# Optimization experiments

Measured on AMD Instinct MI355X. Metric: run time of the kernel, lower is better.

The kernel has to match this reference:

```python
import jax, jax.numpy as jnp
import numpy as np

N_QUBITS = 18
LAYERS = 6
DATA_REUPLOADING = True


def _apply_1q(state, gate, q, n):
    # state: [2^n] complex, gate: [2,2] complex, acts on qubit q (big-endian)
    s = state.reshape(2 ** q, 2, 2 ** (n - q - 1))
    s = jnp.einsum('ab,ibj->iaj', gate, s)
    return s.reshape(-1)


def _apply_cz_adj(state, q, n):
    # CZ on adjacent qubits (q, q+1): flip sign of |..11..> amplitudes
    s = state.reshape(2 ** q, 2, 2, 2 ** (n - q - 2))
    s = s.at[:, 1, 1, :].multiply(-1.0)
    return s.reshape(-1)


def _rx(t):
    c = jnp.cos(t / 2).astype(jnp.complex64)
    s = (-1j * jnp.sin(t / 2)).astype(jnp.complex64)
    return jnp.stack([jnp.stack([c, s]), jnp.stack([s, c])])


def _ry(t):
    c = jnp.cos(t / 2).astype(jnp.complex64)
    s = jnp.sin(t / 2).astype(jnp.complex64)
    return jnp.stack([jnp.stack([c, -s]), jnp.stack([s, c])])


def _rz(t):
    em = jnp.exp(-1j * t.astype(jnp.complex64) / 2)
    ep = jnp.exp(1j * t.astype(jnp.complex64) / 2)
    z = jnp.zeros((), jnp.complex64)
    return jnp.stack([jnp.stack([em, z]), jnp.stack([z, ep])])


def _circuit(x, input_scaling, variational):
    # Hardware-efficient ansatz: RX(data) encoding, RY+RZ variational, CZ chain
    n = N_QUBITS
    state = jnp.zeros(2 ** n, jnp.complex64).at[0].set(1.0)
    for l in range(LAYERS):
        if l == 0 or DATA_REUPLOADING:
            for q in range(n):
                state = _apply_1q(state, _rx(input_scaling[l, q] * x[q]), q, n)
        for q in range(n):
            state = _apply_1q(state, _ry(variational[l, q]), q, n)
        for q in range(n):
            state = _apply_1q(state, _rz(variational[l, n + q]), q, n)
        for q in range(n - 1):
            state = _apply_cz_adj(state, q, n)
    return state


def setup_inputs() -> dict:
    key = jax.random.key(0)
    k1, k2, k3 = jax.random.split(key, 3)
    x1 = jax.random.normal(k1, (N_QUBITS,), jnp.float32)
    x2 = jax.random.normal(k2, (N_QUBITS,), jnp.float32)
    input_scaling = jnp.ones((LAYERS, N_QUBITS), jnp.float32)
    variational = (jax.random.uniform(k3, (LAYERS, 2 * N_QUBITS), jnp.float32)
                   * 2 * np.pi - np.pi)
    return {"x1": x1, "x2": x2, "input_scaling": input_scaling,
            "variational": variational}


def reference(x1, x2, input_scaling, variational):
    psi1 = _circuit(x1, input_scaling, variational)
    psi2 = _circuit(x2, input_scaling, variational)
    # projector |0><0| expectation of U(x2)^dagger U(x1)|0> == |<psi2|psi1>|^2
    ov = jnp.vdot(psi2, psi1)
    return (ov.real ** 2 + ov.imag ** 2).astype(jnp.float32)
```

## Files before the change

### kernel.cpp

```cpp
#include <hip/hip_runtime.h>
#include <math.h>


#define NQ      18
#define NSTATE  (1 << NQ)
#define TPB     256

__device__ __forceinline__ int SW(int i) { return i ^ ((i >> 5) & 31); }

__device__ __forceinline__ float2 cmulf(float2 a, float2 b) {
    return make_float2(a.x * b.x - a.y * b.y, a.x * b.y + a.y * b.x);
}

__device__ __forceinline__ void compose_U(double cx, double sx, double cy,
                                          double sy, double zc, double zs,
                                          float2* up)
{
    double m00r = cy * cx,  m00i =  sy * sx;
    double m01r = -sy * cx, m01i = -cy * sx;
    double m10r = sy * cx,  m10i = -cy * sx;
    double m11r = cy * cx,  m11i = -sy * sx;
    up[0] = make_float2((float)(m00r * zc + m00i * zs), (float)(m00i * zc - m00r * zs));
    up[1] = make_float2((float)(m01r * zc + m01i * zs), (float)(m01i * zc - m01r * zs));
    up[2] = make_float2((float)(m10r * zc - m10i * zs), (float)(m10i * zc + m10r * zs));
    up[3] = make_float2((float)(m11r * zc - m11i * zs), (float)(m11i * zc + m11r * zs));
}

__device__ __forceinline__ void cpair(
    float& a0r, float& a0i, float& a1r, float& a1i,
    float u00r, float u00i, float u01r, float u01i,
    float u10r, float u10i, float u11r, float u11i)
{
    float n0r = u00r * a0r - u00i * a0i + u01r * a1r - u01i * a1i;
    float n0i = u00r * a0i + u00i * a0r + u01r * a1i + u01i * a1r;
    float n1r = u10r * a0r - u10i * a0i + u11r * a1r - u11i * a1i;
    float n1i = u10r * a0i + u10i * a0r + u11r * a1i + u11i * a1r;
    a0r = n0r; a0i = n0i; a1r = n1r; a1i = n1i;
}

template<int RB>
__device__ __forceinline__ void reg_gate8(float (&ar)[8], float (&ai)[8],
                                          const float2* up)
{
    float u00r = up[0].x, u00i = up[0].y, u01r = up[1].x, u01i = up[1].y;
    float u10r = up[2].x, u10i = up[2].y, u11r = up[3].x, u11i = up[3].y;
#pragma unroll
    for (int r = 0; r < 8; ++r) {
        if (r & RB) continue;
        int r1 = r | RB;
        cpair(ar[r], ai[r], ar[r1], ai[r1],
              u00r, u00i, u01r, u01i, u10r, u10i, u11r, u11i);
    }
}

__device__ __forceinline__ void lane_gate8(float (&ar)[8], float (&ai)[8],
                                           const float2* up, int lane, int j)
{
    float u00r = up[0].x, u00i = up[0].y, u01r = up[1].x, u01i = up[1].y;
    float u10r = up[2].x, u10i = up[2].y, u11r = up[3].x, u11i = up[3].y;
    int side = (lane >> j) & 1;
    float car = side ? u11r : u00r, cai = side ? u11i : u00i;
    float cbr = side ? u10r : u01r, cbi = side ? u10i : u01i;
#pragma unroll
    for (int r = 0; r < 8; ++r) {
        float pr = __shfl_xor(ar[r], 1 << j, 64);
        float pi = __shfl_xor(ai[r], 1 << j, 64);
        float mr = ar[r], mi = ai[r];
        ar[r] = car * mr - cai * mi + cbr * pr - cbi * pi;
        ai[r] = car * mi + cai * mr + cbr * pi + cbi * pr;
    }
}

__global__ __launch_bounds__(TPB) void sim_kernel(
    float2* __restrict__ states,
    const float* __restrict__ x1, const float* __restrict__ x2,
    const float* __restrict__ iscale, const float* __restrict__ var,
    double* __restrict__ acc, unsigned* __restrict__ cnt)
{
    __shared__ float sre[2048], sim_[2048];
    __shared__ float2 sUa[5 * 11 * 4];
    __shared__ float2 sUb[5 * 11 * 4];
    __shared__ float2 sDa[6 * 4];
    __shared__ float2 sDb[11 * 4];

    int blk = blockIdx.x, t = threadIdx.x, lane = t & 63, wave = t >> 6;
    int c = blk >> 7, gc = blk & 127;
    const float* xv = c ? x2 : x1;

    if (blk == 0 && t == 0) { acc[0] = 0.0; acc[1] = 0.0; *cnt = 0u; }

    if (t < 110) {
        int which = t >= 55;
        int tt = which ? t - 55 : t;
        int l = tt / 11, w = tt % 11;
        int q = which ? (17 - w) : (10 - w);
        double tx = (double)iscale[l * NQ + q] * (double)xv[q];
        double ty = (double)var[l * 2 * NQ + q];
        double tz = (double)var[l * 2 * NQ + NQ + q];
        double sx, cx, sy, cy, sz, cz;
        sincos(tx * 0.5, &sx, &cx);
        sincos(ty * 0.5, &sy, &cy);
        sincos(tz * 0.5, &sz, &cz);
        compose_U(cx, sx, cy, sy, cz, sz,
                  which ? &sUb[(l * 11 + w) * 4] : &sUa[(l * 11 + w) * 4]);
    } else if (t < 127) {
        int isb = t >= 116;
        int j = isb ? (t - 116) : (t - 110);
        int q = isb ? (17 - j) : (5 - j);
        double d = (double)iscale[5 * NQ + q] * ((double)x1[q] - (double)x2[q]);
        double sn, cs;
        sincos(d * 0.5, &sn, &cs);
        float2* up = isb ? &sDb[j * 4] : &sDa[j * 4];
        up[0] = make_float2((float)cs, 0.f);  up[1] = make_float2(0.f, (float)-sn);
        up[2] = make_float2(0.f, (float)-sn); up[3] = make_float2((float)cs, 0.f);
    }
    __syncthreads();

    float ar[8], ai[8];
    auto W1 = [&](int r) { return r | (wave << 3) | (lane << 5); };
    auto W2 = [&](int r) { return wave | (r << 2) | (lane << 5); };
    auto X1 = [&](int r) { return lane | (wave << 6) | (r << 8); };
    auto X2 = [&](int r) { return lane | (r << 6) | (wave << 9); };
    auto rot = [&](auto from, auto to) {
#pragma unroll
        for (int r = 0; r < 8; ++r) { int s = SW(from(r)); sre[s] = ar[r]; sim_[s] = ai[r]; }
        __syncthreads();
#pragma unroll
        for (int r = 0; r < 8; ++r) { int s = SW(to(r)); ar[r] = sre[s]; ai[r] = sim_[s]; }
    };
    auto Ua = [&](int l, int w) -> const float2* { return &sUa[(l * 11 + w) * 4]; };
    auto Ub = [&](int l, int w) -> const float2* { return &sUb[(l * 11 + w) * 4]; };
    auto czfold = [&](unsigned M, auto gidx) {
#pragma unroll
        for (int r = 0; r < 8; ++r) {
            int i = gidx(r);
            if (__popc(i & (i >> 1) & M) & 1) { ar[r] = -ar[r]; ai[r] = -ai[r]; }
        }
    };
    auto g1_1 = [&](int r) { return W1(r) << 7; };
    auto g1_2 = [&](int r) { return W2(r) << 7; };
    auto g2_1 = [&](int r) { return (gc << 11) | X1(r); };
    auto g2_2 = [&](int r) { return (gc << 11) | X2(r); };

    {
        float2 com = make_float2(1.f, 0.f);
        const float2* u3 = Ua(0, 3); com = cmulf(com, (wave & 1) ? u3[2] : u3[0]);
        const float2* u4 = Ua(0, 4); com = cmulf(com, (wave >> 1) ? u4[2] : u4[0]);
#pragma unroll
        for (int j = 0; j < 6; ++j) {
            const float2* u = Ua(0, 5 + j);
            com = cmulf(com, ((lane >> j) & 1) ? u[2] : u[0]);
        }
        const float2* u0 = Ua(0, 0); const float2* u1 = Ua(0, 1); const float2* u2 = Ua(0, 2);
#pragma unroll
        for (int r = 0; r < 8; ++r) {
            float2 f = cmulf((r & 1) ? u0[2] : u0[0], (r & 2) ? u1[2] : u1[0]);
            f = cmulf(f, (r & 4) ? u2[2] : u2[0]);
            f = cmulf(com, f);
            ar[r] = f.x; ai[r] = f.y;
        }
    }
    czfold(0x1FF80u, g1_1);
    reg_gate8<2>(ar, ai, Ua(1, 1));
    reg_gate8<4>(ar, ai, Ua(1, 2));
#pragma unroll
    for (int j = 0; j < 6; ++j) lane_gate8(ar, ai, Ua(1, 5 + j), lane, j);
    rot(W1, W2);
    reg_gate8<2>(ar, ai, Ua(1, 3));
    reg_gate8<4>(ar, ai, Ua(1, 4));
    czfold(0x1FF00u, g1_2);
    reg_gate8<1>(ar, ai, Ua(2, 2));
    reg_gate8<2>(ar, ai, Ua(2, 3));
    reg_gate8<4>(ar, ai, Ua(2, 4));
#pragma unroll
    for (int j = 0; j < 6; ++j) lane_gate8(ar, ai, Ua(2, 5 + j), lane, j);
    rot(W2, W1);
    czfold(0x1FE00u, g1_1);
#pragma unroll
    for (int j = 0; j < 6; ++j) lane_gate8(ar, ai, Ua(3, 5 + j), lane, j);
    rot(W1, W2);
    reg_gate8<2>(ar, ai, Ua(3, 3));
    reg_gate8<4>(ar, ai, Ua(3, 4));
    czfold(0x1FC00u, g1_2);
    reg_gate8<4>(ar, ai, Ua(4, 4));
#pragma unroll
    for (int j = 0; j < 6; ++j) lane_gate8(ar, ai, Ua(4, 5 + j), lane, j);
    rot(W2, W1);
    czfold(0x1F800u, g1_1);
    if (c == 0) {
#pragma unroll
        for (int j = 0; j < 6; ++j) lane_gate8(ar, ai, &sDa[j * 4], lane, j);
    }
#pragma unroll
    for (int r = 0; r < 8; ++r) { int s = SW(W1(r)); sre[s] = ar[r]; sim_[s] = ai[r]; }
    __syncthreads();
#pragma unroll
    for (int r = 0; r < 8; ++r) {
        int x = X1(r);
        if ((x & 127) == 0) {
            int Wv = (gc << 4) | (x >> 7);
            int s = SW(Wv);
            ar[r] = sre[s]; ai[r] = sim_[s];
        } else { ar[r] = 0.f; ai[r] = 0.f; }
    }
    __syncthreads();

#pragma unroll
    for (int j = 0; j < 6; ++j) lane_gate8(ar, ai, Ub(0, j), lane, j);
    rot(X1, X2);
    reg_gate8<1>(ar, ai, Ub(0, 6));
    czfold(0x7Fu, g2_2);
#pragma unroll
    for (int j = 0; j < 6; ++j) lane_gate8(ar, ai, Ub(1, j), lane, j);
    reg_gate8<1>(ar, ai, Ub(1, 6));
    reg_gate8<2>(ar, ai, Ub(1, 7));
    rot(X2, X1);
    czfold(0xFFu, g2_1);
#pragma unroll
    for (int j = 0; j < 6; ++j) lane_gate8(ar, ai, Ub(2, j), lane, j);
    reg_gate8<1>(ar, ai, Ub(2, 8));
    rot(X1, X2);
    reg_gate8<1>(ar, ai, Ub(2, 6));
    reg_gate8<2>(ar, ai, Ub(2, 7));
    czfold(0x1FFu, g2_2);
#pragma unroll
    for (int j = 0; j < 6; ++j) lane_gate8(ar, ai, Ub(3, j), lane, j);
    reg_gate8<1>(ar, ai, Ub(3, 6));
    reg_gate8<2>(ar, ai, Ub(3, 7));
    reg_gate8<4>(ar, ai, Ub(3, 8));
    rot(X2, X1);
    reg_gate8<2>(ar, ai, Ub(3, 9));
    czfold(0x3FFu, g2_1);
#pragma unroll
    for (int j = 0; j < 6; ++j) lane_gate8(ar, ai, Ub(4, j), lane, j);
    reg_gate8<1>(ar, ai, Ub(4, 8));
    reg_gate8<2>(ar, ai, Ub(4, 9));
    reg_gate8<4>(ar, ai, Ub(4, 10));
    czfold(0x71Fu, g2_1);
    if (c == 0) {
#pragma unroll
        for (int j = 0; j < 5; ++j) lane_gate8(ar, ai, &sDb[j * 4], lane, j);
        reg_gate8<2>(ar, ai, &sDb[9 * 4]);
        reg_gate8<4>(ar, ai, &sDb[10 * 4]);
    }
    rot(X1, X2);
    reg_gate8<1>(ar, ai, Ub(4, 6));
    reg_gate8<2>(ar, ai, Ub(4, 7));
    czfold(0xE0u, g2_2);
    if (c == 0) {
        lane_gate8(ar, ai, &sDb[5 * 4], lane, 5);
        reg_gate8<1>(ar, ai, &sDb[6 * 4]);
        reg_gate8<2>(ar, ai, &sDb[7 * 4]);
        reg_gate8<4>(ar, ai, &sDb[8 * 4]);
    }
    float2* st = states + (size_t)c * NSTATE;
#pragma unroll
    for (int r = 0; r < 8; ++r) {
        int i = (gc << 11) | X2(r);
        st[i] = make_float2(ar[r], ai[r]);
    }
}

__global__ __launch_bounds__(TPB) void dot_kernel(
    const float2* __restrict__ states,
    const float* __restrict__ x1, const float* __restrict__ x2,
    const float* __restrict__ iscale,
    double* __restrict__ acc, unsigned* __restrict__ cnt,
    float* __restrict__ out)
{
    __shared__ double wr[4], wi[4];
    int t = threadIdx.x, lane = t & 63, wave = t >> 6;
    const float2* s1 = states;
    const float2* s2 = states + NSTATE;

    double d = (double)iscale[5 * NQ + 6] * ((double)x1[6] - (double)x2[6]);
    double sn, cs;
    sincos(d * 0.5, &sn, &cs);
    float cf = (float)cs, sf = (float)sn;

    int base = (blockIdx.x * TPB + t) * 4;
    int pbase = base ^ 2048;
    double accr = 0.0, acci = 0.0;
#pragma unroll
    for (int k = 0; k < 4; ++k) {
        float2 p1 = s1[base + k], pp = s1[pbase + k], p2 = s2[base + k];
        float gr = cf * p1.x + sf * pp.y;
        float gi = cf * p1.y - sf * pp.x;
        accr += (double)p2.x * gr + (double)p2.y * gi;
        acci += (double)p2.x * gi - (double)p2.y * gr;
    }
    for (int o = 32; o > 0; o >>= 1) {
        accr += __shfl_down(accr, o, 64);
        acci += __shfl_down(acci, o, 64);
    }
    if (lane == 0) { wr[wave] = accr; wi[wave] = acci; }
    __syncthreads();
    if (t == 0) {
        double br = wr[0] + wr[1] + wr[2] + wr[3];
        double bi = wi[0] + wi[1] + wi[2] + wi[3];
        atomicAdd(&acc[0], br);
        atomicAdd(&acc[1], bi);
        __threadfence();
        unsigned old = atomicAdd(cnt, 1u);
        if (old == gridDim.x - 1) {
            double fr = atomicAdd(&acc[0], 0.0);
            double fi = atomicAdd(&acc[1], 0.0);
            out[0] = (float)(fr * fr + fi * fi);
        }
    }
}

extern "C" void kernel_launch(void* const* d_in, const int* in_sizes, int n_in,
                              void* d_out, int out_size, void* d_ws, size_t ws_size,
                              hipStream_t stream)
{
    const float* x1 = (const float*)d_in[0];
    const float* x2 = (const float*)d_in[1];
    const float* iscale = (const float*)d_in[2];
    const float* var = (const float*)d_in[3];
    float* out = (float*)d_out;

    double*   acc    = (double*)((char*)d_ws + 8192);
    unsigned* cnt    = (unsigned*)((char*)d_ws + 8320);
    float2*   states = (float2*)((char*)d_ws + 16384);

    sim_kernel<<<256, TPB, 0, stream>>>(states, x1, x2, iscale, var, acc, cnt);
    dot_kernel<<<NSTATE / (TPB * 4), TPB, 0, stream>>>(states, x1, x2, iscale,
                                                       acc, cnt, out);
}
```

Before: 100.2 us.

## Fuse overlap reduction into sim kernel via inter-block flag synchronization

```diff
diff --git a/kernel.cpp b/kernel.cpp
--- a/kernel.cpp
+++ b/kernel.cpp
@@ -5,6 +5,7 @@
 #define NQ      18
 #define NSTATE  (1 << NQ)
 #define TPB     256
+#define MAGIC   0x5EED5EEDu
 
 __device__ __forceinline__ int SW(int i) { return i ^ ((i >> 5) & 31); }
 
@@ -23,7 +24,7 @@
     up[0] = make_float2((float)(m00r * zc + m00i * zs), (float)(m00i * zc - m00r * zs));
     up[1] = make_float2((float)(m01r * zc + m01i * zs), (float)(m01i * zc - m01r * zs));
     up[2] = make_float2((float)(m10r * zc - m10i * zs), (float)(m10i * zc + m10r * zs));
-    up[3] = make_float2((float)(m11r * zc - m11i * zs), (float)(m11i * zc + m11r * zs));
+    up[3] = make_float2((float)(m11r * zc + m11i * zs), (float)(m11i * zc + m11r * zs));
 }
 
 __device__ __forceinline__ void cpair(
@@ -75,19 +76,26 @@
     float2* __restrict__ states,
     const float* __restrict__ x1, const float* __restrict__ x2,
     const float* __restrict__ iscale, const float* __restrict__ var,
-    double* __restrict__ acc, unsigned* __restrict__ cnt)
+    double* __restrict__ acc, unsigned* __restrict__ cnt,
+    unsigned* __restrict__ flags, float* __restrict__ out)
 {
     __shared__ float sre[2048], sim_[2048];
     __shared__ float2 sUa[5 * 11 * 4];
     __shared__ float2 sUb[5 * 11 * 4];
     __shared__ float2 sDa[6 * 4];
     __shared__ float2 sDb[11 * 4];
+    __shared__ double wr[4], wi[4];
 
     int blk = blockIdx.x, t = threadIdx.x, lane = t & 63, wave = t >> 6;
     int c = blk >> 7, gc = blk & 127;
     const float* xv = c ? x2 : x1;
 
-    if (blk == 0 && t == 0) { acc[0] = 0.0; acc[1] = 0.0; *cnt = 0u; }
+    if (blk == 0 && t == 0) {
+        acc[0] = 0.0; acc[1] = 0.0; *cnt = 0u;
+        __threadfence();
+        __hip_atomic_store(&flags[128 * 16], MAGIC, __ATOMIC_RELEASE,
+                           __HIP_MEMORY_SCOPE_AGENT);
+    }
 
     if (t < 110) {
         int which = t >= 55;
@@ -101,8 +109,15 @@
         sincos(tx * 0.5, &sx, &cx);
         sincos(ty * 0.5, &sy, &cy);
         sincos(tz * 0.5, &sz, &cz);
-        compose_U(cx, sx, cy, sy, cz, sz,
-                  which ? &sUb[(l * 11 + w) * 4] : &sUa[(l * 11 + w) * 4]);
+        double m00r = cy * cx,  m00i =  sy * sx;
+        double m01r = -sy * cx, m01i = -cy * sx;
+        double m10r = sy * cx,  m10i = -cy * sx;
+        double m11r = cy * cx,  m11i = -sy * sx;
+        float2* up = which ? &sUb[(l * 11 + w) * 4] : &sUa[(l * 11 + w) * 4];
+        up[0] = make_float2((float)(m00r * cz + m00i * sz), (float)(m00i * cz - m00r * sz));
+        up[1] = make_float2((float)(m01r * cz + m01i * sz), (float)(m01i * cz - m01r * sz));
+        up[2] = make_float2((float)(m10r * cz - m10i * sz), (float)(m10i * cz + m10r * sz));
+        up[3] = make_float2((float)(m11r * cz - m11i * sz), (float)(m11i * cz + m11r * sz));
     } else if (t < 127) {
         int isb = t >= 116;
         int j = isb ? (t - 116) : (t - 110);
@@ -252,60 +267,66 @@
         reg_gate8<1>(ar, ai, &sDb[6 * 4]);
         reg_gate8<2>(ar, ai, &sDb[7 * 4]);
         reg_gate8<4>(ar, ai, &sDb[8 * 4]);
-    }
-    float2* st = states + (size_t)c * NSTATE;
-#pragma unroll
-    for (int r = 0; r < 8; ++r) {
-        int i = (gc << 11) | X2(r);
-        st[i] = make_float2(ar[r], ai[r]);
-    }
-}
-
-__global__ __launch_bounds__(TPB) void dot_kernel(
-    const float2* __restrict__ states,
-    const float* __restrict__ x1, const float* __restrict__ x2,
-    const float* __restrict__ iscale,
-    double* __restrict__ acc, unsigned* __restrict__ cnt,
-    float* __restrict__ out)
-{
-    __shared__ double wr[4], wi[4];
-    int t = threadIdx.x, lane = t & 63, wave = t >> 6;
-    const float2* s1 = states;
-    const float2* s2 = states + NSTATE;
-
-    double d = (double)iscale[5 * NQ + 6] * ((double)x1[6] - (double)x2[6]);
-    double sn, cs;
-    sincos(d * 0.5, &sn, &cs);
-    float cf = (float)cs, sf = (float)sn;
-
-    int base = (blockIdx.x * TPB + t) * 4;
-    int pbase = base ^ 2048;
-    double accr = 0.0, acci = 0.0;
-#pragma unroll
-    for (int k = 0; k < 4; ++k) {
-        float2 p1 = s1[base + k], pp = s1[pbase + k], p2 = s2[base + k];
-        float gr = cf * p1.x + sf * pp.y;
-        float gi = cf * p1.y - sf * pp.x;
-        accr += (double)p2.x * gr + (double)p2.y * gi;
-        acci += (double)p2.x * gi - (double)p2.y * gr;
-    }
-    for (int o = 32; o > 0; o >>= 1) {
-        accr += __shfl_down(accr, o, 64);
-        acci += __shfl_down(acci, o, 64);
-    }
-    if (lane == 0) { wr[wave] = accr; wi[wave] = acci; }
-    __syncthreads();
-    if (t == 0) {
-        double br = wr[0] + wr[1] + wr[2] + wr[3];
-        double bi = wi[0] + wi[1] + wi[2] + wi[3];
-        atomicAdd(&acc[0], br);
-        atomicAdd(&acc[1], bi);
-        __threadfence();
-        unsigned old = atomicAdd(cnt, 1u);
-        if (old == gridDim.x - 1) {
-            double fr = atomicAdd(&acc[0], 0.0);
-            double fi = atomicAdd(&acc[1], 0.0);
-            out[0] = (float)(fr * fr + fi * fi);
+
+#pragma unroll
+        for (int r = 0; r < 8; ++r) {
+            int i = (gc << 11) | X2(r);
+            states[i] = make_float2(ar[r], ai[r]);
+        }
+        __syncthreads();
+        if (t == 0) {
+            __threadfence();
+            __hip_atomic_store(&flags[gc * 16], MAGIC, __ATOMIC_RELEASE,
+                               __HIP_MEMORY_SCOPE_AGENT);
+        }
+    } else {
+        double d6 = (double)iscale[5 * NQ + 6] * ((double)x1[6] - (double)x2[6]);
+        double sn6, cs6;
+        sincos(d6 * 0.5, &sn6, &cs6);
+        float cf = (float)cs6, sf = (float)sn6;
+
+        if (t == 0) {
+            while (__hip_atomic_load(&flags[gc * 16], __ATOMIC_ACQUIRE,
+                                     __HIP_MEMORY_SCOPE_AGENT) != MAGIC)
+                __builtin_amdgcn_s_sleep(1);
+            while (__hip_atomic_load(&flags[(gc ^ 1) * 16], __ATOMIC_ACQUIRE,
+                                     __HIP_MEMORY_SCOPE_AGENT) != MAGIC)
+                __builtin_amdgcn_s_sleep(1);
+            while (__hip_atomic_load(&flags[128 * 16], __ATOMIC_ACQUIRE,
+                                     __HIP_MEMORY_SCOPE_AGENT) != MAGIC)
+                __builtin_amdgcn_s_sleep(1);
+        }
+        __syncthreads();
+
+        double accr = 0.0, acci = 0.0;
+#pragma unroll
+        for (int r = 0; r < 8; ++r) {
+            int i = (gc << 11) | X2(r);
+            float2 p1 = states[i];
+            float2 pp = states[i ^ 2048];
+            float gr = cf * p1.x + sf * pp.y;
+            float gi = cf * p1.y - sf * pp.x;
+            accr += (double)ar[r] * gr + (double)ai[r] * gi;
+            acci += (double)ar[r] * gi - (double)ai[r] * gr;
+        }
+        for (int o = 32; o > 0; o >>= 1) {
+            accr += __shfl_down(accr, o, 64);
+            acci += __shfl_down(acci, o, 64);
+        }
+        if (lane == 0) { wr[wave] = accr; wi[wave] = acci; }
+        __syncthreads();
+        if (t == 0) {
+            double br = wr[0] + wr[1] + wr[2] + wr[3];
+            double bi = wi[0] + wi[1] + wi[2] + wi[3];
+            atomicAdd(&acc[0], br);
+            atomicAdd(&acc[1], bi);
+            __threadfence();
+            unsigned old = atomicAdd(cnt, 1u);
+            if (old == 127u) {
+                double fr = atomicAdd(&acc[0], 0.0);
+                double fi = atomicAdd(&acc[1], 0.0);
+                out[0] = (float)(fr * fr + fi * fi);
+            }
         }
     }
 }
@@ -322,9 +343,9 @@
 
     double*   acc    = (double*)((char*)d_ws + 8192);
     unsigned* cnt    = (unsigned*)((char*)d_ws + 8320);
-    float2*   states = (float2*)((char*)d_ws + 16384);
-
-    sim_kernel<<<256, TPB, 0, stream>>>(states, x1, x2, iscale, var, acc, cnt);
-    dot_kernel<<<NSTATE / (TPB * 4), TPB, 0, stream>>>(states, x1, x2, iscale,
-                                                       acc, cnt, out);
-}
+    unsigned* flags  = (unsigned*)((char*)d_ws + 16384);
+    float2*   states = (float2*)((char*)d_ws + 65536);
+
+    sim_kernel<<<256, TPB, 0, stream>>>(states, x1, x2, iscale, var,
+                                        acc, cnt, flags, out);
+}
```

After: 107.3 us. 1.07x slower.
